# Performance work log

Measured on AMD Instinct MI355X. Metric: run time of the kernel, lower is better.

## Reference

```python
import jax, jax.numpy as jnp
import numpy as np

N = 100000
E = 1280000
D = 64


def setup_inputs() -> dict:
    key = jax.random.key(0)
    k1, k2, k3, k4, k5, k6 = jax.random.split(key, 6)
    return {
        "x": jax.random.normal(k1, (N, D), dtype=jnp.float32),
        "w_src": jax.random.normal(k2, (D,), dtype=jnp.float32),
        "w_dst": jax.random.normal(k3, (D,), dtype=jnp.float32),
        "ew": jax.random.normal(k4, (E,), dtype=jnp.float32),
        "src_idx": jax.random.randint(k5, (E,), 0, N, dtype=jnp.int64),
        "dst_idx": jax.random.randint(k6, (E,), 0, N, dtype=jnp.int64),
    }


def reference(x, w_src, w_dst, ew, src_idx, dst_idx):
    # Per-node scalar scores: Linear(emb_dim, 1, bias=False)
    a_src = x @ w_src            # [N]
    a_dst = x @ w_dst            # [N]
    # Edge attention: tanh(a_src[u] + a_dst[v]) * ew  (u_add_v + tanh + scale)
    a = jnp.tanh(a_src[src_idx] + a_dst[dst_idx]) * ew   # [E]
    # Message = a_e * x[src_e]; reduce = scatter-sum over dst (u_mul_e + sum)
    m = a[:, None] * x[src_idx]                           # [E, D]
    h = jax.ops.segment_sum(m, dst_idx, num_segments=N)   # [N, D]
    return h
```

## Files before the change

kernel.cpp:

```cpp
#include <hip/hip_runtime.h>
#include <hip/hip_fp16.h>
#include <math.h>

#define DIM   64
#define SPAN  128
#define SHIFT 7
#define NBIN  256
#define KMAX  1024
#define CAP   3072

__global__ void score_kernel(const float* __restrict__ x,
                             const float* __restrict__ w_src,
                             const float* __restrict__ w_dst,
                             float* __restrict__ a_src,
                             float* __restrict__ a_dst,
                             __half* __restrict__ xh,
                             int N) {
    int gid  = blockIdx.x * blockDim.x + threadIdx.x;
    int node = gid >> 6;
    int lane = threadIdx.x & 63;
    if (node >= N) return;
    float xv = x[(size_t)node * DIM + lane];
    xh[(size_t)node * DIM + lane] = __float2half_rn(xv);
    float s1 = xv * w_src[lane];
    float s2 = xv * w_dst[lane];
    #pragma unroll
    for (int off = 32; off > 0; off >>= 1) {
        s1 += __shfl_down(s1, off, 64);
        s2 += __shfl_down(s2, off, 64);
    }
    if (lane == 0) {
        a_src[node] = s1;
        a_dst[node] = s2;
    }
}

__global__ __launch_bounds__(1024) void hist_coarse(
        const int* __restrict__ dst, int* __restrict__ cnt,
        int E, int N, int K) {
    __shared__ int lh[KMAX];
    int tid = threadIdx.x;
    for (int j = tid; j < K; j += blockDim.x) lh[j] = 0;
    __syncthreads();
    for (int base = blockIdx.x * 1024; base < E; base += NBIN * 1024) {
        int e = base + tid;
        if (e < E) {
            unsigned t = (unsigned)dst[e];
            if (t >= (unsigned)N) t = 0;
            atomicAdd(&lh[t >> SHIFT], 1);
        }
    }
    __syncthreads();
    for (int j = tid; j < K; j += blockDim.x)
        cnt[j * NBIN + blockIdx.x] = lh[j];
}

__global__ __launch_bounds__(512) void scan_part(int* __restrict__ data,
                                                 int* __restrict__ bsum, int n) {
    __shared__ int buf[2][512];
    int tid = threadIdx.x;
    int i = blockIdx.x * 512 + tid;
    int v = (i < n) ? data[i] : 0;
    int sel = 0;
    buf[0][tid] = v;
    __syncthreads();
    for (int off = 1; off < 512; off <<= 1) {
        int nsel = sel ^ 1;
        buf[nsel][tid] = buf[sel][tid] + ((tid >= off) ? buf[sel][tid - off] : 0);
        __syncthreads();
        sel = nsel;
    }
    if (i < n) data[i] = buf[sel][tid] - v;
    if (tid == 511) bsum[blockIdx.x] = buf[sel][511];
}

__global__ __launch_bounds__(512) void scan_top(int* __restrict__ bsum, int NB) {
    __shared__ int buf[2][512];
    int tid = threadIdx.x;
    int v = (tid < NB) ? bsum[tid] : 0;
    int sel = 0;
    buf[0][tid] = v;
    __syncthreads();
    for (int off = 1; off < 512; off <<= 1) {
        int nsel = sel ^ 1;
        buf[nsel][tid] = buf[sel][tid] + ((tid >= off) ? buf[sel][tid - off] : 0);
        __syncthreads();
        sel = nsel;
    }
    if (tid < NB) bsum[tid] = buf[sel][tid] - v;
}

__global__ __launch_bounds__(1024) void binpass_kernel(
        const float* __restrict__ ew,
        const int* __restrict__ src_idx,
        const int* __restrict__ dst_idx,
        const int* __restrict__ moffs,
        const int* __restrict__ bsum,
        unsigned long long* __restrict__ pay,
        int E, int N, int K) {
    __shared__ int lcur[KMAX];
    int tid = threadIdx.x;
    for (int j = tid; j < K; j += blockDim.x) {
        int i = j * NBIN + blockIdx.x;
        lcur[j] = moffs[i] + bsum[i >> 9];
    }
    __syncthreads();
    for (int base = blockIdx.x * 1024; base < E; base += NBIN * 1024) {
        int e = base + tid;
        if (e < E) {
            unsigned s = (unsigned)src_idx[e];
            unsigned t = (unsigned)dst_idx[e];
            if (s >= (unsigned)N) s = 0;
            if (t >= (unsigned)N) t = 0;
            int bk = (int)(t >> SHIFT);
            int pos = atomicAdd(&lcur[bk], 1);
            unsigned rec = (s << 8) | (t & (SPAN - 1));
            pay[pos] = ((unsigned long long)rec << 32) |
                       (unsigned long long)__float_as_uint(ew[e]);
        }
    }
}

__global__ __launch_bounds__(1024) void sort_gather_kernel(
        const __half* __restrict__ xh,
        const float* __restrict__ x32,
        const float* __restrict__ a_src,
        const float* __restrict__ a_dst,
        const unsigned long long* __restrict__ pay,
        const int* __restrict__ moffs,
        const int* __restrict__ bsum,
        float* __restrict__ h,
        int N, int K, int E) {
    __shared__ unsigned long long srec[CAP];
    __shared__ unsigned short sidx[CAP];
    __shared__ int hcnt[SPAN];
    __shared__ int hoff[2][SPAN];
    __shared__ int lcur[SPAN];
    __shared__ int nstart[SPAN];
    int tid = threadIdx.x;
    int b   = blockIdx.x;
    int i0 = b * NBIN;
    int bstart = moffs[i0] + bsum[i0 >> 9];
    int bend;
    if (b == K - 1) bend = E;
    else { int i1 = (b + 1) * NBIN; bend = moffs[i1] + bsum[i1 >> 9]; }
    int cnt = bend - bstart;

    if (cnt <= CAP) {
        if (tid < SPAN) hcnt[tid] = 0;
        __syncthreads();
        for (int i = tid; i < cnt; i += 1024) {
            unsigned long long r = pay[bstart + i];
            srec[i] = r;
            atomicAdd(&hcnt[(int)((r >> 32) & (SPAN - 1))], 1);
        }
        __syncthreads();
        int sel = 0;
        if (tid < SPAN) hoff[0][tid] = hcnt[tid];
        __syncthreads();
        for (int off = 1; off < SPAN; off <<= 1) {
            int nsel = sel ^ 1;
            if (tid < SPAN)
                hoff[nsel][tid] = hoff[sel][tid] +
                                  ((tid >= off) ? hoff[sel][tid - off] : 0);
            __syncthreads();
            sel = nsel;
        }
        if (tid < SPAN) {
            int excl = hoff[sel][tid] - hcnt[tid];
            nstart[tid] = excl;
            lcur[tid]   = excl;
        }
        __syncthreads();
        for (int i = tid; i < cnt; i += 1024) {
            unsigned long long r = srec[i];
            int d = (int)((r >> 32) & (SPAN - 1));
            int pos = atomicAdd(&lcur[d], 1);
            sidx[pos] = (unsigned short)i;
        }
        __syncthreads();
        int lane = tid & 63;
        int wave = tid >> 6;
        for (int d = wave; d < SPAN; d += 16) {
            int node = b * SPAN + d;
            if (node >= N) break;
            int p   = nstart[d];
            int deg = hcnt[d];
            float adt = a_dst[node];
            float acc0 = 0.f, acc1 = 0.f, acc2 = 0.f, acc3 = 0.f;
            for (int c0 = 0; c0 < deg; c0 += 64) {
                int m = deg - c0; if (m > 64) m = 64;
                float aL = 0.f; unsigned sL = 0;
                if (lane < m) {
                    unsigned long long r = srec[sidx[p + c0 + lane]];
                    unsigned s = (unsigned)(r >> 40);
                    if (s >= (unsigned)N) s = 0;
                    aL = tanhf(a_src[s] + adt) * __uint_as_float((unsigned)r);
                    sL = s;
                }
                for (int j = 0; j < m; j += 8) {
                    unsigned s0 = (unsigned)__shfl((int)sL, j + 0, 64);
                    unsigned s1 = (unsigned)__shfl((int)sL, j + 1, 64);
                    unsigned s2 = (unsigned)__shfl((int)sL, j + 2, 64);
                    unsigned s3 = (unsigned)__shfl((int)sL, j + 3, 64);
                    unsigned s4 = (unsigned)__shfl((int)sL, j + 4, 64);
                    unsigned s5 = (unsigned)__shfl((int)sL, j + 5, 64);
                    unsigned s6 = (unsigned)__shfl((int)sL, j + 6, 64);
                    unsigned s7 = (unsigned)__shfl((int)sL, j + 7, 64);
                    float b0 = __shfl(aL, j + 0, 64);
                    float b1 = __shfl(aL, j + 1, 64);
                    float b2 = __shfl(aL, j + 2, 64);
                    float b3 = __shfl(aL, j + 3, 64);
                    float b4 = __shfl(aL, j + 4, 64);
                    float b5 = __shfl(aL, j + 5, 64);
                    float b6 = __shfl(aL, j + 6, 64);
                    float b7 = __shfl(aL, j + 7, 64);
                    float x0 = __half2float(xh[(size_t)s0 * DIM + lane]);
                    float x1 = __half2float(xh[(size_t)s1 * DIM + lane]);
                    float x2 = __half2float(xh[(size_t)s2 * DIM + lane]);
                    float x3 = __half2float(xh[(size_t)s3 * DIM + lane]);
                    float x4 = __half2float(xh[(size_t)s4 * DIM + lane]);
                    float x5 = __half2float(xh[(size_t)s5 * DIM + lane]);
                    float x6 = __half2float(xh[(size_t)s6 * DIM + lane]);
                    float x7 = __half2float(xh[(size_t)s7 * DIM + lane]);
                    acc0 = fmaf(b0, x0, acc0);
                    acc1 = fmaf(b1, x1, acc1);
                    acc2 = fmaf(b2, x2, acc2);
                    acc3 = fmaf(b3, x3, acc3);
                    acc0 = fmaf(b4, x4, acc0);
                    acc1 = fmaf(b5, x5, acc1);
                    acc2 = fmaf(b6, x6, acc2);
                    acc3 = fmaf(b7, x7, acc3);
                }
            }
            h[(size_t)node * DIM + lane] = (acc0 + acc1) + (acc2 + acc3);
        }
    } else {
        for (int j = tid; j < SPAN * DIM; j += 1024) {
            int node = b * SPAN + (j >> 6);
            if (node < N) h[(size_t)node * DIM + (j & 63)] = 0.f;
        }
        __syncthreads();
        for (int i = tid; i < cnt; i += 1024) {
            unsigned long long r = pay[bstart + i];
            unsigned s = (unsigned)(r >> 40);
            if (s >= (unsigned)N) s = 0;
            int node = b * SPAN + (int)((r >> 32) & (SPAN - 1));
            if (node < N) {
                float a = tanhf(a_src[s] + a_dst[node]) *
                          __uint_as_float((unsigned)r);
                for (int k = 0; k < DIM; ++k)
                    atomicAdd(&h[(size_t)node * DIM + k],
                              a * x32[(size_t)s * DIM + k]);
            }
        }
    }
}

__global__ void zero_h_kernel(float* __restrict__ p, int n) {
    int i = blockIdx.x * blockDim.x + threadIdx.x;
    if (i < n) p[i] = 0.f;
}

__global__ void edge_kernel_atomic(const float* __restrict__ x,
                                   const float* __restrict__ ew,
                                   const int* __restrict__ src_idx,
                                   const int* __restrict__ dst_idx,
                                   const float* __restrict__ a_src,
                                   const float* __restrict__ a_dst,
                                   float* __restrict__ h,
                                   int E) {
    int gid  = blockIdx.x * blockDim.x + threadIdx.x;
    int e    = gid >> 6;
    int lane = threadIdx.x & 63;
    if (e >= E) return;
    int s = src_idx[e];
    int t = dst_idx[e];
    float a  = tanhf(a_src[s] + a_dst[t]) * ew[e];
    float xv = x[(size_t)s * DIM + lane];
    atomicAdd(&h[(size_t)t * DIM + lane], a * xv);
}

__global__ void score_only_kernel(const float* __restrict__ x,
                                  const float* __restrict__ w_src,
                                  const float* __restrict__ w_dst,
                                  float* __restrict__ a_src,
                                  float* __restrict__ a_dst,
                                  int N) {
    int gid  = blockIdx.x * blockDim.x + threadIdx.x;
    int node = gid >> 6;
    int lane = threadIdx.x & 63;
    if (node >= N) return;
    float xv = x[(size_t)node * DIM + lane];
    float s1 = xv * w_src[lane];
    float s2 = xv * w_dst[lane];
    #pragma unroll
    for (int off = 32; off > 0; off >>= 1) {
        s1 += __shfl_down(s1, off, 64);
        s2 += __shfl_down(s2, off, 64);
    }
    if (lane == 0) {
        a_src[node] = s1;
        a_dst[node] = s2;
    }
}

extern "C" void kernel_launch(void* const* d_in, const int* in_sizes, int n_in,
                              void* d_out, int out_size, void* d_ws, size_t ws_size,
                              hipStream_t stream) {
    const float* x     = (const float*)d_in[0];
    const float* w_src = (const float*)d_in[1];
    const float* w_dst = (const float*)d_in[2];
    const float* ew    = (const float*)d_in[3];
    const int*   src   = (const int*)d_in[4];
    const int*   dst   = (const int*)d_in[5];
    float* h = (float*)d_out;

    int N = in_sizes[0] / DIM;
    int E = in_sizes[3];

    int K    = (N + SPAN - 1) / SPAN;
    int Ntot = K * NBIN;
    int NBs  = (Ntot + 511) / 512;

    float* a_src  = (float*)d_ws;
    float* a_dst  = a_src + N;
    int*   moffs  = (int*)(a_dst + N);
    int*   bsum   = moffs + Ntot + 1;
    size_t head_bytes = ((size_t)(2 * N) + (size_t)Ntot + 1 + (size_t)NBs) * 4;
    size_t pay_off = (head_bytes + 15) & ~(size_t)15;
    unsigned long long* pay = (unsigned long long*)((char*)d_ws + pay_off);
    size_t xh_off = pay_off + (size_t)E * 8;
    __half* xh = (__half*)((char*)d_ws + xh_off);
    size_t need = xh_off + (size_t)N * DIM * 2;

    int score_blocks = (N + 3) / 4;

    if (ws_size < need || K > KMAX || NBs > 512 || N >= (1 << 24)) {
        score_only_kernel<<<score_blocks, 256, 0, stream>>>(x, w_src, w_dst,
                                                            a_src, a_dst, N);
        int ob = (out_size + 255) / 256;
        zero_h_kernel<<<ob, 256, 0, stream>>>(h, out_size);
        int edge_blocks = (E + 3) / 4;
        edge_kernel_atomic<<<edge_blocks, 256, 0, stream>>>(x, ew, src, dst,
                                                            a_src, a_dst, h, E);
        return;
    }

    score_kernel<<<score_blocks, 256, 0, stream>>>(x, w_src, w_dst,
                                                   a_src, a_dst, xh, N);
    hist_coarse<<<NBIN, 1024, 0, stream>>>(dst, moffs, E, N, K);
    scan_part<<<NBs, 512, 0, stream>>>(moffs, bsum, Ntot);
    scan_top<<<1, 512, 0, stream>>>(bsum, NBs);
    binpass_kernel<<<NBIN, 1024, 0, stream>>>(ew, src, dst, moffs, bsum,
                                              pay, E, N, K);
    sort_gather_kernel<<<K, 1024, 0, stream>>>(xh, x, a_src, a_dst, pay,
                                               moffs, bsum, h, N, K, E);
}
```

Before: 192.5 us.

## Fuse score and histogram kernels, precompute edge attention in binning, vectorize gather

Merges the per-node score and fp16-conversion kernel with the coarse dst histogram into one 256-block kernel, removing a launch. The tanh attention coefficient is now computed once per edge in the binning pass and stored in the payload instead of the raw edge weight, so the gather kernel no longer reads a_src/a_dst. The gather loop is restructured so each half-wave handles alternating edges with half2 loads and eight float2 accumulators, combined at the end with a cross-half shuffle. The fused kernel has less parallelism for the score phase, and the binning pass picks up random a_src/a_dst gathers.

```diff
diff --git a/kernel.cpp b/kernel.cpp
--- a/kernel.cpp
+++ b/kernel.cpp
@@ -9,49 +9,45 @@
 #define KMAX  1024
 #define CAP   3072
 
-__global__ void score_kernel(const float* __restrict__ x,
-                             const float* __restrict__ w_src,
-                             const float* __restrict__ w_dst,
-                             float* __restrict__ a_src,
-                             float* __restrict__ a_dst,
-                             __half* __restrict__ xh,
-                             int N) {
-    int gid  = blockIdx.x * blockDim.x + threadIdx.x;
-    int node = gid >> 6;
-    int lane = threadIdx.x & 63;
-    if (node >= N) return;
-    float xv = x[(size_t)node * DIM + lane];
-    xh[(size_t)node * DIM + lane] = __float2half_rn(xv);
-    float s1 = xv * w_src[lane];
-    float s2 = xv * w_dst[lane];
-    #pragma unroll
-    for (int off = 32; off > 0; off >>= 1) {
-        s1 += __shfl_down(s1, off, 64);
-        s2 += __shfl_down(s2, off, 64);
-    }
-    if (lane == 0) {
-        a_src[node] = s1;
-        a_dst[node] = s2;
-    }
-}
-
-__global__ __launch_bounds__(1024) void hist_coarse(
-        const int* __restrict__ dst, int* __restrict__ cnt,
-        int E, int N, int K) {
+__global__ __launch_bounds__(1024) void score_hist_kernel(
+        const float* __restrict__ x,
+        const float* __restrict__ w_src,
+        const float* __restrict__ w_dst,
+        float* __restrict__ a_src,
+        float* __restrict__ a_dst,
+        __half* __restrict__ xh,
+        const int* __restrict__ dst,
+        int* __restrict__ cnt,
+        int N, int E, int K) {
     __shared__ int lh[KMAX];
     int tid = threadIdx.x;
-    for (int j = tid; j < K; j += blockDim.x) lh[j] = 0;
-    __syncthreads();
-    for (int base = blockIdx.x * 1024; base < E; base += NBIN * 1024) {
-        int e = base + tid;
-        if (e < E) {
-            unsigned t = (unsigned)dst[e];
-            if (t >= (unsigned)N) t = 0;
-            atomicAdd(&lh[t >> SHIFT], 1);
-        }
-    }
-    __syncthreads();
-    for (int j = tid; j < K; j += blockDim.x)
+    for (int j = tid; j < K; j += 1024) lh[j] = 0;
+    int lane = tid & 63;
+    int wv = (blockIdx.x << 4) + (tid >> 6);
+    int nw = gridDim.x << 4;
+    for (int node = wv; node < N; node += nw) {
+        float xv = x[(size_t)node * DIM + lane];
+        xh[(size_t)node * DIM + lane] = __float2half_rn(xv);
+        float s1 = xv * w_src[lane];
+        float s2 = xv * w_dst[lane];
+        #pragma unroll
+        for (int off = 32; off > 0; off >>= 1) {
+            s1 += __shfl_down(s1, off, 64);
+            s2 += __shfl_down(s2, off, 64);
+        }
+        if (lane == 0) {
+            a_src[node] = s1;
+            a_dst[node] = s2;
+        }
+    }
+    __syncthreads();
+    for (int e = blockIdx.x * 1024 + tid; e < E; e += gridDim.x * 1024) {
+        unsigned t = (unsigned)dst[e];
+        if (t >= (unsigned)N) t = 0;
+        atomicAdd(&lh[t >> SHIFT], 1);
+    }
+    __syncthreads();
+    for (int j = tid; j < K; j += 1024)
         cnt[j * NBIN + blockIdx.x] = lh[j];
 }
 
@@ -94,13 +90,15 @@
         const float* __restrict__ ew,
         const int* __restrict__ src_idx,
         const int* __restrict__ dst_idx,
+        const float* __restrict__ a_src,
+        const float* __restrict__ a_dst,
         const int* __restrict__ moffs,
         const int* __restrict__ bsum,
         unsigned long long* __restrict__ pay,
         int E, int N, int K) {
     __shared__ int lcur[KMAX];
     int tid = threadIdx.x;
-    for (int j = tid; j < K; j += blockDim.x) {
+    for (int j = tid; j < K; j += 1024) {
         int i = j * NBIN + blockIdx.x;
         lcur[j] = moffs[i] + bsum[i >> 9];
     }
@@ -112,11 +110,12 @@
             unsigned t = (unsigned)dst_idx[e];
             if (s >= (unsigned)N) s = 0;
             if (t >= (unsigned)N) t = 0;
+            float a = tanhf(a_src[s] + a_dst[t]) * ew[e];
             int bk = (int)(t >> SHIFT);
             int pos = atomicAdd(&lcur[bk], 1);
             unsigned rec = (s << 8) | (t & (SPAN - 1));
             pay[pos] = ((unsigned long long)rec << 32) |
-                       (unsigned long long)__float_as_uint(ew[e]);
+                       (unsigned long long)__float_as_uint(a);
         }
     }
 }
@@ -124,8 +123,6 @@
 __global__ __launch_bounds__(1024) void sort_gather_kernel(
         const __half* __restrict__ xh,
         const float* __restrict__ x32,
-        const float* __restrict__ a_src,
-        const float* __restrict__ a_dst,
         const unsigned long long* __restrict__ pay,
         const int* __restrict__ moffs,
         const int* __restrict__ bsum,
@@ -181,59 +178,74 @@
         __syncthreads();
         int lane = tid & 63;
         int wave = tid >> 6;
+        int half = lane >> 5;
+        int hl   = lane & 31;
+        const __half2* xh2 = (const __half2*)xh;
         for (int d = wave; d < SPAN; d += 16) {
             int node = b * SPAN + d;
             if (node >= N) break;
             int p   = nstart[d];
             int deg = hcnt[d];
-            float adt = a_dst[node];
-            float acc0 = 0.f, acc1 = 0.f, acc2 = 0.f, acc3 = 0.f;
-            for (int c0 = 0; c0 < deg; c0 += 64) {
-                int m = deg - c0; if (m > 64) m = 64;
-                float aL = 0.f; unsigned sL = 0;
-                if (lane < m) {
-                    unsigned long long r = srec[sidx[p + c0 + lane]];
-                    unsigned s = (unsigned)(r >> 40);
-                    if (s >= (unsigned)N) s = 0;
-                    aL = tanhf(a_src[s] + adt) * __uint_as_float((unsigned)r);
-                    sL = s;
-                }
-                for (int j = 0; j < m; j += 8) {
-                    unsigned s0 = (unsigned)__shfl((int)sL, j + 0, 64);
-                    unsigned s1 = (unsigned)__shfl((int)sL, j + 1, 64);
-                    unsigned s2 = (unsigned)__shfl((int)sL, j + 2, 64);
-                    unsigned s3 = (unsigned)__shfl((int)sL, j + 3, 64);
-                    unsigned s4 = (unsigned)__shfl((int)sL, j + 4, 64);
-                    unsigned s5 = (unsigned)__shfl((int)sL, j + 5, 64);
-                    unsigned s6 = (unsigned)__shfl((int)sL, j + 6, 64);
-                    unsigned s7 = (unsigned)__shfl((int)sL, j + 7, 64);
-                    float b0 = __shfl(aL, j + 0, 64);
-                    float b1 = __shfl(aL, j + 1, 64);
-                    float b2 = __shfl(aL, j + 2, 64);
-                    float b3 = __shfl(aL, j + 3, 64);
-                    float b4 = __shfl(aL, j + 4, 64);
-                    float b5 = __shfl(aL, j + 5, 64);
-                    float b6 = __shfl(aL, j + 6, 64);
-                    float b7 = __shfl(aL, j + 7, 64);
-                    float x0 = __half2float(xh[(size_t)s0 * DIM + lane]);
-                    float x1 = __half2float(xh[(size_t)s1 * DIM + lane]);
-                    float x2 = __half2float(xh[(size_t)s2 * DIM + lane]);
-                    float x3 = __half2float(xh[(size_t)s3 * DIM + lane]);
-                    float x4 = __half2float(xh[(size_t)s4 * DIM + lane]);
-                    float x5 = __half2float(xh[(size_t)s5 * DIM + lane]);
-                    float x6 = __half2float(xh[(size_t)s6 * DIM + lane]);
-                    float x7 = __half2float(xh[(size_t)s7 * DIM + lane]);
-                    acc0 = fmaf(b0, x0, acc0);
-                    acc1 = fmaf(b1, x1, acc1);
-                    acc2 = fmaf(b2, x2, acc2);
-                    acc3 = fmaf(b3, x3, acc3);
-                    acc0 = fmaf(b4, x4, acc0);
-                    acc1 = fmaf(b5, x5, acc1);
-                    acc2 = fmaf(b6, x6, acc2);
-                    acc3 = fmaf(b7, x7, acc3);
-                }
+            int m   = deg - 1;
+            float2 acc0 = {0.f, 0.f}, acc1 = {0.f, 0.f};
+            float2 acc2 = {0.f, 0.f}, acc3 = {0.f, 0.f};
+            float2 acc4 = {0.f, 0.f}, acc5 = {0.f, 0.f};
+            float2 acc6 = {0.f, 0.f}, acc7 = {0.f, 0.f};
+            for (int c = 0; c < deg; c += 16) {
+                int j0 = c + 0  + half; int j1 = c + 2  + half;
+                int j2 = c + 4  + half; int j3 = c + 6  + half;
+                int j4 = c + 8  + half; int j5 = c + 10 + half;
+                int j6 = c + 12 + half; int j7 = c + 14 + half;
+                unsigned long long r0 = srec[sidx[p + (j0 <= m ? j0 : m)]];
+                unsigned long long r1 = srec[sidx[p + (j1 <= m ? j1 : m)]];
+                unsigned long long r2 = srec[sidx[p + (j2 <= m ? j2 : m)]];
+                unsigned long long r3 = srec[sidx[p + (j3 <= m ? j3 : m)]];
+                unsigned long long r4 = srec[sidx[p + (j4 <= m ? j4 : m)]];
+                unsigned long long r5 = srec[sidx[p + (j5 <= m ? j5 : m)]];
+                unsigned long long r6 = srec[sidx[p + (j6 <= m ? j6 : m)]];
+                unsigned long long r7 = srec[sidx[p + (j7 <= m ? j7 : m)]];
+                float a0 = (j0 <= m) ? __uint_as_float((unsigned)r0) : 0.f;
+                float a1 = (j1 <= m) ? __uint_as_float((unsigned)r1) : 0.f;
+                float a2 = (j2 <= m) ? __uint_as_float((unsigned)r2) : 0.f;
+                float a3 = (j3 <= m) ? __uint_as_float((unsigned)r3) : 0.f;
+                float a4 = (j4 <= m) ? __uint_as_float((unsigned)r4) : 0.f;
+                float a5 = (j5 <= m) ? __uint_as_float((unsigned)r5) : 0.f;
+                float a6 = (j6 <= m) ? __uint_as_float((unsigned)r6) : 0.f;
+                float a7 = (j7 <= m) ? __uint_as_float((unsigned)r7) : 0.f;
+                unsigned s0 = (unsigned)(r0 >> 40); if (s0 >= (unsigned)N) s0 = 0;
+                unsigned s1 = (unsigned)(r1 >> 40); if (s1 >= (unsigned)N) s1 = 0;
+                unsigned s2 = (unsigned)(r2 >> 40); if (s2 >= (unsigned)N) s2 = 0;
+                unsigned s3 = (unsigned)(r3 >> 40); if (s3 >= (unsigned)N) s3 = 0;
+                unsigned s4 = (unsigned)(r4 >> 40); if (s4 >= (unsigned)N) s4 = 0;
+                unsigned s5 = (unsigned)(r5 >> 40); if (s5 >= (unsigned)N) s5 = 0;
+                unsigned s6 = (unsigned)(r6 >> 40); if (s6 >= (unsigned)N) s6 = 0;
+                unsigned s7 = (unsigned)(r7 >> 40); if (s7 >= (unsigned)N) s7 = 0;
+                float2 x0 = __half22float2(xh2[(size_t)s0 * 32 + hl]);
+                float2 x1 = __half22float2(xh2[(size_t)s1 * 32 + hl]);
+                float2 x2 = __half22float2(xh2[(size_t)s2 * 32 + hl]);
+                float2 x3 = __half22float2(xh2[(size_t)s3 * 32 + hl]);
+                float2 x4 = __half22float2(xh2[(size_t)s4 * 32 + hl]);
+                float2 x5 = __half22float2(xh2[(size_t)s5 * 32 + hl]);
+                float2 x6 = __half22float2(xh2[(size_t)s6 * 32 + hl]);
+                float2 x7 = __half22float2(xh2[(size_t)s7 * 32 + hl]);
+                acc0.x = fmaf(a0, x0.x, acc0.x); acc0.y = fmaf(a0, x0.y, acc0.y);
+                acc1.x = fmaf(a1, x1.x, acc1.x); acc1.y = fmaf(a1, x1.y, acc1.y);
+                acc2.x = fmaf(a2, x2.x, acc2.x); acc2.y = fmaf(a2, x2.y, acc2.y);
+                acc3.x = fmaf(a3, x3.x, acc3.x); acc3.y = fmaf(a3, x3.y, acc3.y);
+                acc4.x = fmaf(a4, x4.x, acc4.x); acc4.y = fmaf(a4, x4.y, acc4.y);
+                acc5.x = fmaf(a5, x5.x, acc5.x); acc5.y = fmaf(a5, x5.y, acc5.y);
+                acc6.x = fmaf(a6, x6.x, acc6.x); acc6.y = fmaf(a6, x6.y, acc6.y);
+                acc7.x = fmaf(a7, x7.x, acc7.x); acc7.y = fmaf(a7, x7.y, acc7.y);
             }
-            h[(size_t)node * DIM + lane] = (acc0 + acc1) + (acc2 + acc3);
+            float2 acc;
+            acc.x = ((acc0.x + acc1.x) + (acc2.x + acc3.x)) +
+                    ((acc4.x + acc5.x) + (acc6.x + acc7.x));
+            acc.y = ((acc0.y + acc1.y) + (acc2.y + acc3.y)) +
+                    ((acc4.y + acc5.y) + (acc6.y + acc7.y));
+            acc.x += __shfl_xor(acc.x, 32, 64);
+            acc.y += __shfl_xor(acc.y, 32, 64);
+            if (half == 0)
+                ((float2*)h)[(size_t)node * 32 + hl] = acc;
         }
     } else {
         for (int j = tid; j < SPAN * DIM; j += 1024) {
@@ -246,13 +258,11 @@
             unsigned s = (unsigned)(r >> 40);
             if (s >= (unsigned)N) s = 0;
             int node = b * SPAN + (int)((r >> 32) & (SPAN - 1));
-            if (node < N) {
-                float a = tanhf(a_src[s] + a_dst[node]) *
-                          __uint_as_float((unsigned)r);
+            float a = __uint_as_float((unsigned)r);
+            if (node < N)
                 for (int k = 0; k < DIM; ++k)
                     atomicAdd(&h[(size_t)node * DIM + k],
                               a * x32[(size_t)s * DIM + k]);
-            }
         }
     }
 }
@@ -334,9 +344,8 @@
     __half* xh = (__half*)((char*)d_ws + xh_off);
     size_t need = xh_off + (size_t)N * DIM * 2;
 
-    int score_blocks = (N + 3) / 4;
-
     if (ws_size < need || K > KMAX || NBs > 512 || N >= (1 << 24)) {
+        int score_blocks = (N + 3) / 4;
         score_only_kernel<<<score_blocks, 256, 0, stream>>>(x, w_src, w_dst,
                                                             a_src, a_dst, N);
         int ob = (out_size + 255) / 256;
@@ -347,13 +356,12 @@
         return;
     }
 
-    score_kernel<<<score_blocks, 256, 0, stream>>>(x, w_src, w_dst,
-                                                   a_src, a_dst, xh, N);
-    hist_coarse<<<NBIN, 1024, 0, stream>>>(dst, moffs, E, N, K);
+    score_hist_kernel<<<NBIN, 1024, 0, stream>>>(x, w_src, w_dst, a_src, a_dst,
+                                                 xh, dst, moffs, N, E, K);
     scan_part<<<NBs, 512, 0, stream>>>(moffs, bsum, Ntot);
     scan_top<<<1, 512, 0, stream>>>(bsum, NBs);
-    binpass_kernel<<<NBIN, 1024, 0, stream>>>(ew, src, dst, moffs, bsum,
-                                              pay, E, N, K);
-    sort_gather_kernel<<<K, 1024, 0, stream>>>(xh, x, a_src, a_dst, pay,
-                                               moffs, bsum, h, N, K, E);
-}
+    binpass_kernel<<<NBIN, 1024, 0, stream>>>(ew, src, dst, a_src, a_dst,
+                                              moffs, bsum, pay, E, N, K);
+    sort_gather_kernel<<<K, 1024, 0, stream>>>(xh, x, pay, moffs, bsum,
+                                               h, N, K, E);
+}
```

New measurement: 188.8 us. About the same (-1.9%).
